# Performance work log

Hardware: AMD Instinct MI355X
Metric: run time of the kernel (lower is better)

The kernel has to match this reference:

```python
import jax, jax.numpy as jnp
import numpy as np

B, H, Q, S, D = 2, 16, 2048, 2048, 64  # bs, n_heads, q_len, seq_len, head_dim


def setup_inputs() -> dict:
    key = jax.random.key(0)
    k1, k2, k3, k4 = jax.random.split(key, 4)
    q = jax.random.normal(k1, (B, H, Q, D), jnp.float32)
    k = jax.random.normal(k2, (B, H, D, S), jnp.float32)  # K pre-transposed as in module docstring
    v = jax.random.normal(k3, (B, H, S, D), jnp.float32)
    prev = jax.random.normal(k4, (B, H, Q, S), jnp.float32) * 0.1  # residual attention from prev layer
    causal = jnp.triu(jnp.ones((S, S), bool), 1)
    attn_mask = jnp.where(causal, jnp.float32(-1e9), jnp.float32(0.0))[None]  # [1,S,S] additive mask
    key_padding_mask = jnp.zeros((B, S), bool)  # no padded keys (avoids fully-masked rows)
    scale = jnp.asarray(D ** -0.5, jnp.float32)  # learnable scale (lsa=True)
    return {"q": q, "k": k, "v": v, "scale": scale, "prev": prev,
            "attn_mask": attn_mask, "key_padding_mask": key_padding_mask, "cross": 0}


def reference(q, k, v, scale, prev, attn_mask, key_padding_mask, cross):
    # cross=False branch of _ScaledDotProductAttention (attn_dropout=0.0 -> identity)
    scores = jnp.einsum('bhqd,bhds->bhqs', q, k) * scale  # [B,H,Q,S]
    scores = scores + prev + attn_mask                    # residual attn + additive float mask
    # key padding: masked_fill with -inf (applied twice in source; idempotent)
    scores = jnp.where(key_padding_mask[:, None, None, :], -jnp.inf, scores)
    attn = jax.nn.softmax(scores, axis=-1)                # [B,H,Q,S]
    out = jnp.einsum('bhqs,bhsd->bhqd', attn, v)          # [B,H,Q,D]
    return out, attn, scores  # res_attention=True returns (output, attn_weights, attn_scores)
```

## Files before the change

kernel.cpp:

```cpp
#include <hip/hip_runtime.h>

#define B_  2
#define H_  16
#define QL  2048
#define SL  2048
#define DH  64
#define TQ  16
#define TS  256
#define NT  256

__global__ __launch_bounds__(NT, 4) void attn_fused(
    const float* __restrict__ qp, const float* __restrict__ kp,
    const float* __restrict__ vp, const float* __restrict__ scalep,
    const float* __restrict__ prevp,
    float* __restrict__ outp, float* __restrict__ attnp, float* __restrict__ scoresp)
{
    const int qt   = (int)(gridDim.x - 1) - (int)blockIdx.x;
    const int bh   = blockIdx.y;
    const int tid  = threadIdx.x;
    const int lane = tid & 63;
    const int wv   = tid >> 6;
    const int r0   = qt * TQ;

    __shared__ float q_lds[TQ][DH];
    __shared__ float e_lds[TQ][TS];
    __shared__ float l_lds[TQ];
    __shared__ float linv_lds[TQ];

    const float scale = scalep[0];

    const float* qbase = qp + ((long)bh * QL + r0) * DH;
    const float* kbase = kp + (long)bh * DH * SL;
    const float* vbase = vp + (long)bh * (long)SL * DH;
    const float* pbase = prevp  + ((long)bh * QL + r0) * (long)SL;
    float* sbase = scoresp + ((long)bh * QL + r0) * (long)SL;
    float* abase = attnp   + ((long)bh * QL + r0) * (long)SL;
    float* obase = outp    + ((long)bh * QL + r0) * DH;

    for (int i = tid; i < TQ * DH; i += NT)
        ((float*)q_lds)[i] = qbase[i];
    __syncthreads();

    float l_acc[4] = {0.f, 0.f, 0.f, 0.f};
    float o_acc[4] = {0.f, 0.f, 0.f, 0.f};

    const int jmax   = r0 + TQ;
    const int ntiles = (jmax + TS - 1) / TS;

    for (int t = 0; t < ntiles; t++) {
        const int s0 = t * TS;
        const float* krow = kbase + s0 + lane * 4;

        float acc[4][4];
        #pragma unroll
        for (int i = 0; i < 4; i++)
            #pragma unroll
            for (int c = 0; c < 4; c++) acc[i][c] = 0.f;

        #pragma unroll 2
        for (int d4 = 0; d4 < DH; d4 += 4) {
            float kq[4][4];
            #pragma unroll
            for (int dd = 0; dd < 4; dd++) {
                const float4 tkv = *(const float4*)(krow + (long)(d4 + dd) * SL);
                kq[dd][0] = tkv.x; kq[dd][1] = tkv.y; kq[dd][2] = tkv.z; kq[dd][3] = tkv.w;
            }
            #pragma unroll
            for (int i = 0; i < 4; i++) {
                const float4 qv = *(const float4*)(&q_lds[4 * wv + i][d4]);
                #pragma unroll
                for (int c = 0; c < 4; c++) {
                    acc[i][c] = fmaf(qv.x, kq[0][c], acc[i][c]);
                    acc[i][c] = fmaf(qv.y, kq[1][c], acc[i][c]);
                    acc[i][c] = fmaf(qv.z, kq[2][c], acc[i][c]);
                    acc[i][c] = fmaf(qv.w, kq[3][c], acc[i][c]);
                }
            }
        }

        __syncthreads();

        #pragma unroll
        for (int i = 0; i < 4; i++) {
            const int r   = 4 * wv + i;
            const int row = r0 + r;
            const long off = (long)r * SL + s0 + lane * 4;
            const float4 pv = *(const float4*)(pbase + off);
            float sc[4], ev[4];
            const float pvv[4] = {pv.x, pv.y, pv.z, pv.w};
            #pragma unroll
            for (int c = 0; c < 4; c++) {
                const int s = s0 + lane * 4 + c;
                float v = fmaf(acc[i][c], scale, pvv[c]);
                if (s > row) v -= 1e9f;
                sc[c] = v;
                ev[c] = (s > row) ? 0.f : __expf(v);
                l_acc[i] += ev[c];
            }
            *(float4*)(sbase + off) = make_float4(sc[0], sc[1], sc[2], sc[3]);
            *(float4*)(&e_lds[r][lane * 4]) = make_float4(ev[0], ev[1], ev[2], ev[3]);
        }
        __syncthreads();

        const int send = min(TS, jmax - s0);
        const float* vrow = vbase + (long)s0 * DH + lane;
        for (int sl = 0; sl < send; sl += 4) {
            float vv[4];
            #pragma unroll
            for (int u = 0; u < 4; u++) vv[u] = vrow[(long)(sl + u) * DH];
            #pragma unroll
            for (int j = 0; j < 4; j++) {
                const float4 e4 = *(const float4*)(&e_lds[4 * wv + j][sl]);
                o_acc[j] = fmaf(e4.x, vv[0], o_acc[j]);
                o_acc[j] = fmaf(e4.y, vv[1], o_acc[j]);
                o_acc[j] = fmaf(e4.z, vv[2], o_acc[j]);
                o_acc[j] = fmaf(e4.w, vv[3], o_acc[j]);
            }
        }
    }

    #pragma unroll
    for (int i = 0; i < 4; i++) {
        float lv = l_acc[i];
        for (int off = 32; off > 0; off >>= 1) lv += __shfl_down(lv, off);
        if (lane == 0) l_lds[4 * wv + i] = lv;
    }
    __syncthreads();
    if (tid < TQ) linv_lds[tid] = 1.0f / l_lds[tid];
    __syncthreads();

    #pragma unroll
    for (int j = 0; j < 4; j++) {
        const int r = 4 * wv + j;
        obase[(long)r * DH + lane] = o_acc[j] * linv_lds[r];
    }

    const int cols1 = ntiles * TS;
    for (int r = 0; r < TQ; r++) {
        const float rinv = linv_lds[r];
        const long rowoff = (long)r * SL;
        for (int s4 = tid; s4 < cols1 / 4; s4 += NT) {
            const float4 sc = *(const float4*)(sbase + rowoff + (long)s4 * 4);
            float4 a;
            a.x = __expf(sc.x) * rinv;
            a.y = __expf(sc.y) * rinv;
            a.z = __expf(sc.z) * rinv;
            a.w = __expf(sc.w) * rinv;
            *(float4*)(abase + rowoff + (long)s4 * 4) = a;
        }
    }

    const float4 negbig = make_float4(-1e9f, -1e9f, -1e9f, -1e9f);
    const float4 zero4  = make_float4(0.f, 0.f, 0.f, 0.f);
    for (int r = 0; r < TQ; r++) {
        const long rowoff = (long)r * SL;
        for (int s4 = cols1 / 4 + tid; s4 < SL / 4; s4 += NT) {
            *(float4*)(sbase + rowoff + (long)s4 * 4) = negbig;
            *(float4*)(abase + rowoff + (long)s4 * 4) = zero4;
        }
    }
}

extern "C" void kernel_launch(void* const* d_in, const int* in_sizes, int n_in,
                              void* d_out, int out_size, void* d_ws, size_t ws_size,
                              hipStream_t stream) {
    const float* q     = (const float*)d_in[0];
    const float* k     = (const float*)d_in[1];
    const float* v     = (const float*)d_in[2];
    const float* scale = (const float*)d_in[3];
    const float* prev  = (const float*)d_in[4];

    float* outp    = (float*)d_out;
    float* attnp   = outp + (long)B_ * H_ * QL * DH;
    float* scoresp = attnp + (long)B_ * H_ * QL * (long)SL;

    dim3 grid(QL / TQ, B_ * H_);
    attn_fused<<<grid, NT, 0, stream>>>(q, k, v, scale, prev, outp, attnp, scoresp);
}
```

Before: 2.156 ms.

## Make each wavefront own its rows, dropping block barriers and vectorizing PV

Each wavefront now owns four query rows end to end: it loads its own Q rows, writes and reads its own exp rows in shared memory, and reduces row sums with xor-shuffles. This removes every __syncthreads from the tile loop and the epilogue. The P·V loop is reorganized so lanes form four groups of 16, each doing float4 V loads over a strided subset of keys, with a shuffle reduction across groups at the end. The prev tile is also prefetched before the QK product to hide its load latency, at the cost of extra registers from the 4x4 output accumulators.

```diff
diff --git a/kernel.cpp b/kernel.cpp
--- a/kernel.cpp
+++ b/kernel.cpp
@@ -21,11 +21,11 @@
     const int lane = tid & 63;
     const int wv   = tid >> 6;
     const int r0   = qt * TQ;
+    const int g    = lane >> 4;
+    const int dl   = lane & 15;
 
     __shared__ float q_lds[TQ][DH];
     __shared__ float e_lds[TQ][TS];
-    __shared__ float l_lds[TQ];
-    __shared__ float linv_lds[TQ];
 
     const float scale = scalep[0];
 
@@ -37,20 +37,31 @@
     float* abase = attnp   + ((long)bh * QL + r0) * (long)SL;
     float* obase = outp    + ((long)bh * QL + r0) * DH;
 
-    for (int i = tid; i < TQ * DH; i += NT)
-        ((float*)q_lds)[i] = qbase[i];
-    __syncthreads();
+    {
+        const int qr = 4 * wv + g;
+        const float4 qv = *(const float4*)(qbase + (long)qr * DH + 4 * dl);
+        *(float4*)(&q_lds[qr][4 * dl]) = qv;
+    }
 
     float l_acc[4] = {0.f, 0.f, 0.f, 0.f};
-    float o_acc[4] = {0.f, 0.f, 0.f, 0.f};
+    float o_acc[4][4];
+    #pragma unroll
+    for (int i = 0; i < 4; i++)
+        #pragma unroll
+        for (int c = 0; c < 4; c++) o_acc[i][c] = 0.f;
 
     const int jmax   = r0 + TQ;
     const int ntiles = (jmax + TS - 1) / TS;
 
     for (int t = 0; t < ntiles; t++) {
         const int s0 = t * TS;
+
+        float4 pf[4];
+        #pragma unroll
+        for (int i = 0; i < 4; i++)
+            pf[i] = *(const float4*)(pbase + (long)(4 * wv + i) * SL + s0 + lane * 4);
+
         const float* krow = kbase + s0 + lane * 4;
-
         float acc[4][4];
         #pragma unroll
         for (int i = 0; i < 4; i++)
@@ -78,16 +89,13 @@
             }
         }
 
-        __syncthreads();
-
         #pragma unroll
         for (int i = 0; i < 4; i++) {
             const int r   = 4 * wv + i;
             const int row = r0 + r;
             const long off = (long)r * SL + s0 + lane * 4;
-            const float4 pv = *(const float4*)(pbase + off);
             float sc[4], ev[4];
-            const float pvv[4] = {pv.x, pv.y, pv.z, pv.w};
+            const float pvv[4] = {pf[i].x, pf[i].y, pf[i].z, pf[i].w};
             #pragma unroll
             for (int c = 0; c < 4; c++) {
                 const int s = s0 + lane * 4 + c;
@@ -100,61 +108,74 @@
             *(float4*)(sbase + off) = make_float4(sc[0], sc[1], sc[2], sc[3]);
             *(float4*)(&e_lds[r][lane * 4]) = make_float4(ev[0], ev[1], ev[2], ev[3]);
         }
-        __syncthreads();
-
-        const int send = min(TS, jmax - s0);
-        const float* vrow = vbase + (long)s0 * DH + lane;
-        for (int sl = 0; sl < send; sl += 4) {
-            float vv[4];
-            #pragma unroll
-            for (int u = 0; u < 4; u++) vv[u] = vrow[(long)(sl + u) * DH];
-            #pragma unroll
-            for (int j = 0; j < 4; j++) {
-                const float4 e4 = *(const float4*)(&e_lds[4 * wv + j][sl]);
-                o_acc[j] = fmaf(e4.x, vv[0], o_acc[j]);
-                o_acc[j] = fmaf(e4.y, vv[1], o_acc[j]);
-                o_acc[j] = fmaf(e4.z, vv[2], o_acc[j]);
-                o_acc[j] = fmaf(e4.w, vv[3], o_acc[j]);
-            }
-        }
-    }
-
+
+        const int send   = min(TS, jmax - s0);
+        const int ksteps = send >> 2;
+        const float* vptr = vbase + ((long)s0 + g) * DH + 4 * dl;
+        #pragma unroll 4
+        for (int k = 0; k < ksteps; k++) {
+            const float4 vv = *(const float4*)(vptr + (long)(4 * k) * DH);
+            #pragma unroll
+            for (int i = 0; i < 4; i++) {
+                const float ee = e_lds[4 * wv + i][4 * k + g];
+                o_acc[i][0] = fmaf(ee, vv.x, o_acc[i][0]);
+                o_acc[i][1] = fmaf(ee, vv.y, o_acc[i][1]);
+                o_acc[i][2] = fmaf(ee, vv.z, o_acc[i][2]);
+                o_acc[i][3] = fmaf(ee, vv.w, o_acc[i][3]);
+            }
+        }
+    }
+
+    float rinv[4];
     #pragma unroll
     for (int i = 0; i < 4; i++) {
         float lv = l_acc[i];
-        for (int off = 32; off > 0; off >>= 1) lv += __shfl_down(lv, off);
-        if (lane == 0) l_lds[4 * wv + i] = lv;
-    }
-    __syncthreads();
-    if (tid < TQ) linv_lds[tid] = 1.0f / l_lds[tid];
-    __syncthreads();
-
-    #pragma unroll
-    for (int j = 0; j < 4; j++) {
-        const int r = 4 * wv + j;
-        obase[(long)r * DH + lane] = o_acc[j] * linv_lds[r];
+        #pragma unroll
+        for (int off = 32; off > 0; off >>= 1) lv += __shfl_xor(lv, off);
+        rinv[i] = 1.0f / lv;
+    }
+
+    #pragma unroll
+    for (int i = 0; i < 4; i++)
+        #pragma unroll
+        for (int c = 0; c < 4; c++) {
+            float v = o_acc[i][c];
+            v += __shfl_xor(v, 16);
+            v += __shfl_xor(v, 32);
+            o_acc[i][c] = v;
+        }
+
+    if (g == 0) {
+        #pragma unroll
+        for (int i = 0; i < 4; i++) {
+            const int r = 4 * wv + i;
+            float4 o4;
+            o4.x = o_acc[i][0] * rinv[i];
+            o4.y = o_acc[i][1] * rinv[i];
+            o4.z = o_acc[i][2] * rinv[i];
+            o4.w = o_acc[i][3] * rinv[i];
+            *(float4*)(obase + (long)r * DH + 4 * dl) = o4;
+        }
     }
 
     const int cols1 = ntiles * TS;
-    for (int r = 0; r < TQ; r++) {
-        const float rinv = linv_lds[r];
+    #pragma unroll
+    for (int i = 0; i < 4; i++) {
+        const int r  = 4 * wv + i;
+        const float ri = rinv[i];
         const long rowoff = (long)r * SL;
-        for (int s4 = tid; s4 < cols1 / 4; s4 += NT) {
+        for (int s4 = lane; s4 < cols1 / 4; s4 += 64) {
             const float4 sc = *(const float4*)(sbase + rowoff + (long)s4 * 4);
             float4 a;
-            a.x = __expf(sc.x) * rinv;
-            a.y = __expf(sc.y) * rinv;
-            a.z = __expf(sc.z) * rinv;
-            a.w = __expf(sc.w) * rinv;
+            a.x = __expf(sc.x) * ri;
+            a.y = __expf(sc.y) * ri;
+            a.z = __expf(sc.z) * ri;
+            a.w = __expf(sc.w) * ri;
             *(float4*)(abase + rowoff + (long)s4 * 4) = a;
         }
-    }
-
-    const float4 negbig = make_float4(-1e9f, -1e9f, -1e9f, -1e9f);
-    const float4 zero4  = make_float4(0.f, 0.f, 0.f, 0.f);
-    for (int r = 0; r < TQ; r++) {
-        const long rowoff = (long)r * SL;
-        for (int s4 = cols1 / 4 + tid; s4 < SL / 4; s4 += NT) {
+        const float4 negbig = make_float4(-1e9f, -1e9f, -1e9f, -1e9f);
+        const float4 zero4  = make_float4(0.f, 0.f, 0.f, 0.f);
+        for (int s4 = cols1 / 4 + lane; s4 < SL / 4; s4 += 64) {
             *(float4*)(sbase + rowoff + (long)s4 * 4) = negbig;
             *(float4*)(abase + rowoff + (long)s4 * 4) = zero4;
         }
```

After: 2.003 ms. -7.1%, faster.
